# Kernel tuning notes

Hardware: AMD Instinct MI355X
Metric: run time of the kernel (lower is better)

The kernel has to match this reference:

```python
import jax, jax.numpy as jnp
import numpy as np

B, S, D, H = 8, 1024, 768, 12
DH = D // H
EPS = 1e-5
NEG = -1e9


def _layernorm(x, g, b):
    mu = jnp.mean(x, axis=-1, keepdims=True)
    var = jnp.mean((x - mu) ** 2, axis=-1, keepdims=True)
    return (x - mu) * jax.lax.rsqrt(var + EPS) * g + b


def setup_inputs() -> dict:
    key = jax.random.key(0)
    ks = jax.random.split(key, 20)
    sc = 0.02
    x = jax.random.normal(ks[0], (B, S, D), dtype=jnp.float32)
    src_mask = jax.random.randint(ks[1], (B, S), 0, 2) > 0
    # weights stored as (in, out): y = x @ W + b (same math as torch x @ W.T + b)
    Wq = jax.random.normal(ks[2], (D, D), jnp.float32) * sc
    bq = jnp.zeros((D,), jnp.float32)
    Wk = jax.random.normal(ks[3], (D, D), jnp.float32) * sc
    bk = jnp.zeros((D,), jnp.float32)
    Wv = jax.random.normal(ks[4], (D, D), jnp.float32) * sc
    bv = jnp.zeros((D,), jnp.float32)
    Wo = jax.random.normal(ks[5], (D, D), jnp.float32) * sc
    bo = jnp.zeros((D,), jnp.float32)
    g1 = jnp.ones((D,), jnp.float32)
    be1 = jnp.zeros((D,), jnp.float32)
    W1 = jax.random.normal(ks[6], (D, 2 * D), jnp.float32) * sc
    b1 = jnp.zeros((2 * D,), jnp.float32)
    W2 = jax.random.normal(ks[7], (2 * D, D), jnp.float32) * sc
    b2 = jnp.zeros((D,), jnp.float32)
    g2 = jnp.ones((D,), jnp.float32)
    be2 = jnp.zeros((D,), jnp.float32)
    return dict(x=x, src_mask=src_mask, Wq=Wq, bq=bq, Wk=Wk, bk=bk, Wv=Wv, bv=bv,
                Wo=Wo, bo=bo, g1=g1, be1=be1, W1=W1, b1=b1, W2=W2, b2=b2,
                g2=g2, be2=be2)


def reference(x, src_mask, Wq, bq, Wk, bk, Wv, bv, Wo, bo, g1, be1, W1, b1, W2, b2, g2, be2):
    # QKV projections, split into heads: [B, S, H, DH]
    q = (x @ Wq + bq).reshape(B, S, H, DH)
    k = (x @ Wk + bk).reshape(B, S, H, DH)
    v = (x @ Wv + bv).reshape(B, S, H, DH)
    # scores [B, H, S, S]; scale by sqrt(head_dim) as in original
    scores = jnp.einsum('bqhd,bkhd->bhqk', q, k) / np.sqrt(DH).astype(np.float32)
    # additive key mask broadcast over heads and queries
    mask = jnp.where(src_mask[:, None, None, :], 0.0, NEG).astype(scores.dtype)
    A = jax.nn.softmax(scores + mask, axis=-1)
    ctx = jnp.einsum('bhqk,bkhd->bqhd', A, v).reshape(B, S, D)
    attn_out = ctx @ Wo + bo + x
    h = _layernorm(attn_out, g1, be1)
    ff = jax.nn.relu(h @ W1 + b1) @ W2 + b2
    out = _layernorm(ff + h, g2, be2)
    return out
```

## Files before the change

kernel.cpp:

```cpp
#include <hip/hip_runtime.h>
#include <cstdint>
#include <cstddef>

typedef unsigned short u16;
typedef __attribute__((ext_vector_type(8))) __bf16 bf16x8;
typedef __attribute__((ext_vector_type(4))) float floatx4;

#define Bz 8
#define Sz 1024
#define Dz 768
#define Hz 12
#define DHz 64

__device__ __forceinline__ u16 f2b(float f) {
  unsigned u = __float_as_uint(f);
  return (u16)((u + 0x7fffu + ((u >> 16) & 1u)) >> 16);
}

__device__ __forceinline__ bf16x8 ld8(const u16* p) {
  union { uint4 u; bf16x8 b; } t;
  t.u = *reinterpret_cast<const uint4*>(p);
  return t.b;
}

__device__ __forceinline__ void load_lds16(const u16* g, u16* l) {
  __builtin_amdgcn_global_load_lds(
      (const __attribute__((address_space(1))) unsigned int*)g,
      (__attribute__((address_space(3))) unsigned int*)l, 16, 0, 0);
}

__global__ __launch_bounds__(256) void cvt4(const float* __restrict__ src,
                                            u16* __restrict__ dst, int n4) {
  int i = blockIdx.x * 256 + threadIdx.x;
  if (i >= n4) return;
  float4 v = reinterpret_cast<const float4*>(src)[i];
  union { u16 s[4]; uint2 u; } t;
  t.s[0] = f2b(v.x); t.s[1] = f2b(v.y); t.s[2] = f2b(v.z); t.s[3] = f2b(v.w);
  reinterpret_cast<uint2*>(dst)[i] = t.u;
}

__global__ __launch_bounds__(256)
void wtrans(const float* __restrict__ s0, const float* __restrict__ s1,
            const float* __restrict__ s2, u16* __restrict__ dst,
            int K, int N, int srcN) {
  __shared__ float T[32][33];
  const int tx = threadIdx.x & 31, ty = threadIdx.x >> 5;
  const int n0 = blockIdx.x * 32, k0 = blockIdx.y * 32;
  const int n = n0 + tx;
  const float* src = s0;
  int nn = n;
  if (s1 && n >= 1536) { src = s2; nn = n - 1536; }
  else if (s1 && n >= 768) { src = s1; nn = n - 768; }
#pragma unroll
  for (int i = 0; i < 4; ++i)
    T[ty + i * 8][tx] = src[(size_t)(k0 + ty + i * 8) * srcN + nn];
  __syncthreads();
#pragma unroll
  for (int i = 0; i < 4; ++i)
    dst[(size_t)(n0 + ty + i * 8) * K + k0 + tx] = f2b(T[tx][ty + i * 8]);
}

template <int EPI>
__global__ __launch_bounds__(256, 4)
void gemm_k(const u16* __restrict__ A, const u16* __restrict__ Bt,
            int M, int N, int K,
            const float* __restrict__ bias0, const float* __restrict__ bias1,
            const float* __restrict__ bias2, const float* __restrict__ resid,
            float* __restrict__ outF, u16* __restrict__ outB,
            u16* __restrict__ qO, u16* __restrict__ kO, u16* __restrict__ vtO) {
  __shared__ __align__(16) u16 As[2][128 * 32];
  __shared__ __align__(16) u16 Bs[2][128 * 32];
  const int tid = threadIdx.x;
  const int lane = tid & 63, wave = tid >> 6;
  const int l15 = lane & 15, quad = lane >> 4;
  const int m0 = blockIdx.y * 128, n0 = blockIdx.x * 128;
  const int wm = (wave >> 1) * 64, wn = (wave & 1) * 64;

  floatx4 acc[4][4];
#pragma unroll
  for (int i = 0; i < 4; ++i)
#pragma unroll
    for (int j = 0; j < 4; ++j) acc[i][j] = {0.f, 0.f, 0.f, 0.f};

  const int srow = lane >> 2;
  const int scol = (lane & 3) * 8;
  const u16* pA = A + (size_t)(m0 + wave * 32 + srow) * K + scol;
  const u16* pB = Bt + (size_t)(n0 + wave * 32 + srow) * K + scol;

#pragma unroll
  for (int j = 0; j < 2; ++j) {
    load_lds16(pA + (size_t)(j * 16) * K, &As[0][(wave * 2 + j) * 512]);
    load_lds16(pB + (size_t)(j * 16) * K, &Bs[0][(wave * 2 + j) * 512]);
  }

  const int NIT = K >> 5;
  for (int i = 0; i < NIT; ++i) {
    const int cur = i & 1;
    asm volatile("s_waitcnt vmcnt(0)" ::: "memory");
    __builtin_amdgcn_s_barrier();
    bf16x8 af[4], bf[4];
#pragma unroll
    for (int ii = 0; ii < 4; ++ii)
      af[ii] = ld8(&As[cur][(wm + ii * 16 + l15) * 32 + quad * 8]);
#pragma unroll
    for (int j = 0; j < 4; ++j)
      bf[j] = ld8(&Bs[cur][(wn + j * 16 + l15) * 32 + quad * 8]);
    __builtin_amdgcn_sched_barrier(0);
    if (i + 1 < NIT) {
      const int k1 = (i + 1) << 5;
#pragma unroll
      for (int j = 0; j < 2; ++j) {
        load_lds16(pA + (size_t)(j * 16) * K + k1, &As[cur ^ 1][(wave * 2 + j) * 512]);
        load_lds16(pB + (size_t)(j * 16) * K + k1, &Bs[cur ^ 1][(wave * 2 + j) * 512]);
      }
    }
#pragma unroll
    for (int ii = 0; ii < 4; ++ii)
#pragma unroll
      for (int j = 0; j < 4; ++j)
        acc[ii][j] = __builtin_amdgcn_mfma_f32_16x16x32_bf16(af[ii], bf[j],
                                                             acc[ii][j], 0, 0, 0);
  }

#pragma unroll
  for (int i = 0; i < 4; ++i) {
    int mbase = m0 + wm + i * 16 + quad * 4;
#pragma unroll
    for (int j = 0; j < 4; ++j) {
      int n = n0 + wn + j * 16 + l15;
#pragma unroll
      for (int r = 0; r < 4; ++r) {
        int mm = mbase + r;
        float v = acc[i][j][r];
        if (EPI == 0) {
          if (n < 768) {
            v += bias0[n];
            qO[(size_t)mm * 768 + n] = f2b(v);
          } else if (n < 1536) {
            v += bias1[n - 768];
            kO[(size_t)mm * 768 + (n - 768)] = f2b(v);
          } else {
            int d = n - 1536;
            v += bias2[d];
            int hh = d >> 6, dh = d & 63;
            int bb = mm >> 10, ss = mm & 1023;
            vtO[((size_t)(bb * Hz + hh) * DHz + dh) * Sz + ss] = f2b(v);
          }
        } else if (EPI == 1) {
          v += bias0[n] + resid[(size_t)mm * N + n];
          outF[(size_t)mm * N + n] = v;
        } else {
          v += bias0[n];
          v = fmaxf(v, 0.f);
          outB[(size_t)mm * N + n] = f2b(v);
        }
      }
    }
  }
}

__global__ __launch_bounds__(256, 3)
void attn_k(const u16* __restrict__ q, const u16* __restrict__ kbuf,
            const u16* __restrict__ vt, const int* __restrict__ mask,
            u16* __restrict__ ctx) {
  __shared__ float addend[Sz];
  __shared__ __align__(16) u16 Ks[128 * 64];
  __shared__ __align__(16) u16 Vs[64 * 128];
  __shared__ __align__(16) u16 P[4][16][132];
  const int tid = threadIdx.x;
  const int wave = tid >> 6, lane = tid & 63;
  const int l15 = lane & 15, quad = lane >> 4;
  const int bq = blockIdx.x;
  const int b = blockIdx.y / Hz, h = blockIdx.y % Hz;

  for (int s = tid; s < Sz; s += 256)
    addend[s] = mask[b * Sz + s] ? 0.f : -1e9f;

  const int qrow = bq * 64 + wave * 16 + l15;
  const u16* qp = q + (size_t)(b * Sz + qrow) * Dz + h * DHz;
  const bf16x8 fq0 = ld8(qp + quad * 8);
  const bf16x8 fq1 = ld8(qp + 32 + quad * 8);

  const int kchunk = (lane & 7) ^ (lane >> 3);
  const int l7 = l15 & 7;
  const int s0q = quad ^ l7;

  float m_l = -1e30f, l_l = 0.f;
  floatx4 o[4];
#pragma unroll
  for (int nt = 0; nt < 4; ++nt) o[nt] = {0.f, 0.f, 0.f, 0.f};

  const size_t vbase = (size_t)(b * Hz + h) * DHz * Sz;

  for (int kt = 0; kt < Sz / 128; ++kt) {
    __syncthreads();
#pragma unroll
    for (int j = 0; j < 4; ++j) {
      const int key = wave * 32 + j * 8 + (lane >> 3);
      load_lds16(kbuf + (size_t)(b * Sz + kt * 128 + key) * Dz + h * DHz +
                     kchunk * 8,
                 Ks + wave * 2048 + j * 512);
      const int dh = wave * 16 + j * 4 + (lane >> 4);
      const int vchunk = (lane & 15) ^ (dh & 7);
      load_lds16(vt + vbase + (size_t)dh * Sz + kt * 128 + vchunk * 8,
                 Vs + wave * 2048 + j * 512);
    }
    __syncthreads();

    floatx4 z[8];
#pragma unroll
    for (int t = 0; t < 8; ++t) {
      const int krow = t * 16 + l15;
      bf16x8 fk0 = ld8(&Ks[krow * 64 + s0q * 8]);
      bf16x8 fk1 = ld8(&Ks[krow * 64 + (s0q ^ 4) * 8]);
      floatx4 zz = {0.f, 0.f, 0.f, 0.f};
      zz = __builtin_amdgcn_mfma_f32_16x16x32_bf16(fk0, fq0, zz, 0, 0, 0);
      zz = __builtin_amdgcn_mfma_f32_16x16x32_bf16(fk1, fq1, zz, 0, 0, 0);
      const float4 ad =
          *reinterpret_cast<const float4*>(&addend[kt * 128 + t * 16 + quad * 4]);
      z[t][0] = zz[0] * 0.125f + ad.x;
      z[t][1] = zz[1] * 0.125f + ad.y;
      z[t][2] = zz[2] * 0.125f + ad.z;
      z[t][3] = zz[3] * 0.125f + ad.w;
    }
    float mx = z[0][0];
#pragma unroll
    for (int t = 0; t < 8; ++t)
#pragma unroll
      for (int r = 0; r < 4; ++r) mx = fmaxf(mx, z[t][r]);
    mx = fmaxf(mx, __shfl_xor(mx, 16, 64));
    mx = fmaxf(mx, __shfl_xor(mx, 32, 64));
    const float nm = fmaxf(m_l, mx);
    const float alpha = __expf(m_l - nm);
    m_l = nm;
    float su = 0.f;
#pragma unroll
    for (int t = 0; t < 8; ++t) {
      union { u16 s[4]; uint2 u; } pk;
#pragma unroll
      for (int r = 0; r < 4; ++r) {
        float p = __expf(z[t][r] - nm);
        su += p;
        pk.s[r] = f2b(p);
      }
      *reinterpret_cast<uint2*>(&P[wave][l15][t * 16 + quad * 4]) = pk.u;
    }
    su += __shfl_xor(su, 16, 64);
    su += __shfl_xor(su, 32, 64);
    l_l = l_l * alpha + su;
    float av[4];
#pragma unroll
    for (int r = 0; r < 4; ++r) av[r] = __shfl(alpha, quad * 4 + r, 64);
#pragma unroll
    for (int nt = 0; nt < 4; ++nt)
#pragma unroll
      for (int r = 0; r < 4; ++r) o[nt][r] *= av[r];
    bf16x8 ap[4];
#pragma unroll
    for (int c = 0; c < 4; ++c)
      ap[c] = ld8(&P[wave][l15][c * 32 + quad * 8]);
#pragma unroll
    for (int nt = 0; nt < 4; ++nt) {
#pragma unroll
      for (int c = 0; c < 4; ++c) {
        bf16x8 bv =
            ld8(&Vs[(nt * 16 + l15) * 128 + (((c * 4 + quad) ^ l7) * 8)]);
        o[nt] = __builtin_amdgcn_mfma_f32_16x16x32_bf16(ap[c], bv, o[nt], 0, 0, 0);
      }
    }
  }

  const float linv = 1.f / l_l;
  float lv[4];
#pragma unroll
  for (int r = 0; r < 4; ++r) lv[r] = __shfl(linv, quad * 4 + r, 64);
  const int qr = bq * 64 + wave * 16 + quad * 4;
#pragma unroll
  for (int nt = 0; nt < 4; ++nt)
#pragma unroll
    for (int r = 0; r < 4; ++r) {
      float v = o[nt][r] * lv[r];
      ctx[(size_t)(b * Sz + qr + r) * Dz + h * DHz + nt * 16 + l15] = f2b(v);
    }
}

__global__ __launch_bounds__(256)
void ln_k(const float* __restrict__ in, const float* __restrict__ g,
          const float* __restrict__ be, float* __restrict__ outF,
          u16* __restrict__ outB) {
  const int row = blockIdx.x;
  const float* x = in + (size_t)row * Dz;
  const int tid = threadIdx.x;
  float v0 = x[tid], v1 = x[tid + 256], v2 = x[tid + 512];
  float s = v0 + v1 + v2;
  float s2 = v0 * v0 + v1 * v1 + v2 * v2;
#pragma unroll
  for (int off = 1; off < 64; off <<= 1) {
    s += __shfl_xor(s, off, 64);
    s2 += __shfl_xor(s2, off, 64);
  }
  __shared__ float red[8];
  int wave = tid >> 6, lane = tid & 63;
  if (lane == 0) { red[wave] = s; red[4 + wave] = s2; }
  __syncthreads();
  s = red[0] + red[1] + red[2] + red[3];
  s2 = red[4] + red[5] + red[6] + red[7];
  const float mu = s * (1.f / 768.f);
  const float rstd = rsqrtf(s2 * (1.f / 768.f) - mu * mu + 1e-5f);
  float vv[3] = {v0, v1, v2};
#pragma unroll
  for (int e = 0; e < 3; ++e) {
    int col = tid + e * 256;
    float y = (vv[e] - mu) * rstd * g[col] + be[col];
    outF[(size_t)row * Dz + col] = y;
    if (outB) outB[(size_t)row * Dz + col] = f2b(y);
  }
}

extern "C" void kernel_launch(void* const* d_in, const int* in_sizes, int n_in,
                              void* d_out, int out_size, void* d_ws,
                              size_t ws_size, hipStream_t stream) {
  const float* x   = (const float*)d_in[0];
  const int*   msk = (const int*)d_in[1];
  const float* Wq  = (const float*)d_in[2];
  const float* bq  = (const float*)d_in[3];
  const float* Wk  = (const float*)d_in[4];
  const float* bk  = (const float*)d_in[5];
  const float* Wv  = (const float*)d_in[6];
  const float* bv  = (const float*)d_in[7];
  const float* Wo  = (const float*)d_in[8];
  const float* bo  = (const float*)d_in[9];
  const float* g1  = (const float*)d_in[10];
  const float* be1 = (const float*)d_in[11];
  const float* W1  = (const float*)d_in[12];
  const float* b1  = (const float*)d_in[13];
  const float* W2  = (const float*)d_in[14];
  const float* b2  = (const float*)d_in[15];
  const float* g2  = (const float*)d_in[16];
  const float* be2 = (const float*)d_in[17];
  float* out = (float*)d_out;

  char* ws = (char*)d_ws;
  u16*   xb    = (u16*)(ws + 0);
  u16*   wqkvb = (u16*)(ws + 12582912);
  u16*   wob   = (u16*)(ws + 16121856);
  u16*   w1b   = (u16*)(ws + 17301504);
  u16*   w2b   = (u16*)(ws + 19660800);
  u16*   qb    = (u16*)(ws + 22020096);
  u16*   kb    = (u16*)(ws + 34603008);
  u16*   vtb   = (u16*)(ws + 47185920);
  u16*   ctx   = (u16*)(ws + 59768832);
  float* att   = (float*)(ws + 72351744);
  float* hf    = (float*)(ws + 97517568);
  u16*   hb    = (u16*)(ws + 122683392);
  u16*   f1    = (u16*)(ws + 47185920);
  float* yy    = (float*)(ws + 22020096);

  cvt4<<<6291456 / 4 / 256, 256, 0, stream>>>(x, xb, 6291456 / 4);
  wtrans<<<dim3(2304 / 32, 768 / 32), 256, 0, stream>>>(Wq, Wk, Wv, wqkvb, 768,
                                                        2304, 768);
  wtrans<<<dim3(24, 24), 256, 0, stream>>>(Wo, nullptr, nullptr, wob, 768, 768,
                                           768);
  wtrans<<<dim3(48, 24), 256, 0, stream>>>(W1, nullptr, nullptr, w1b, 768, 1536,
                                           1536);
  wtrans<<<dim3(24, 48), 256, 0, stream>>>(W2, nullptr, nullptr, w2b, 1536, 768,
                                           768);

  gemm_k<0><<<dim3(2304 / 128, 8192 / 128), 256, 0, stream>>>(
      xb, wqkvb, 8192, 2304, 768, bq, bk, bv, nullptr, nullptr, nullptr, qb, kb,
      vtb);
  attn_k<<<dim3(Sz / 64, Bz * Hz), 256, 0, stream>>>(qb, kb, vtb, msk, ctx);
  gemm_k<1><<<dim3(768 / 128, 8192 / 128), 256, 0, stream>>>(
      ctx, wob, 8192, 768, 768, bo, nullptr, nullptr, x, att, nullptr, nullptr,
      nullptr, nullptr);
  ln_k<<<8192, 256, 0, stream>>>(att, g1, be1, hf, hb);
  gemm_k<2><<<dim3(1536 / 128, 8192 / 128), 256, 0, stream>>>(
      hb, w1b, 8192, 1536, 768, b1, nullptr, nullptr, nullptr, nullptr, f1,
      nullptr, nullptr, nullptr);
  gemm_k<1><<<dim3(768 / 128, 8192 / 128), 256, 0, stream>>>(
      f1, w2b, 8192, 768, 1536, b2, nullptr, nullptr, hf, yy, nullptr, nullptr,
      nullptr, nullptr);
  ln_k<<<8192, 256, 0, stream>>>(yy, g2, be2, out, nullptr);
}
```

Baseline: 387.9 us.

## Triple-buffer GEMM LDS tiles, swizzle LDS columns, and remap workgroups for XCD locality

The GEMM kernel moves from double to triple buffering. It prefetches two K-steps ahead and waits on a partial vmcnt, so global-to-LDS loads can overlap more MFMA work. LDS column chunks are XOR-swizzled on both the write and read side to cut bank conflicts. Both the GEMM and attention kernels remap the linear block id with a stride-8 swizzle so neighbouring tiles land on the same XCD and share L2. In exchange, LDS use per block rises and launch bounds drop to 3 blocks per CU, which may lower occupancy. The vmcnt(4) wait count must exactly match the number of outstanding loads issued per step.

```diff
diff --git a/kernel.cpp b/kernel.cpp
--- a/kernel.cpp
+++ b/kernel.cpp
@@ -61,19 +61,26 @@
 }
 
 template <int EPI>
-__global__ __launch_bounds__(256, 4)
+__global__ __launch_bounds__(256, 3)
 void gemm_k(const u16* __restrict__ A, const u16* __restrict__ Bt,
             int M, int N, int K,
             const float* __restrict__ bias0, const float* __restrict__ bias1,
             const float* __restrict__ bias2, const float* __restrict__ resid,
             float* __restrict__ outF, u16* __restrict__ outB,
             u16* __restrict__ qO, u16* __restrict__ kO, u16* __restrict__ vtO) {
-  __shared__ __align__(16) u16 As[2][128 * 32];
-  __shared__ __align__(16) u16 Bs[2][128 * 32];
+  __shared__ __align__(16) u16 As[3][128 * 32];
+  __shared__ __align__(16) u16 Bs[3][128 * 32];
   const int tid = threadIdx.x;
   const int lane = tid & 63, wave = tid >> 6;
   const int l15 = lane & 15, quad = lane >> 4;
-  const int m0 = blockIdx.y * 128, n0 = blockIdx.x * 128;
+
+  const int nx = gridDim.x;
+  const int nwg = nx * gridDim.y;
+  const int lin = blockIdx.y * nx + blockIdx.x;
+  const int swz = (lin & 7) * (nwg >> 3) + (lin >> 3);
+  const int bx = swz % nx, by = swz / nx;
+
+  const int m0 = by * 128, n0 = bx * 128;
   const int wm = (wave >> 1) * 64, wn = (wave & 1) * 64;
 
   floatx4 acc[4][4];
@@ -83,43 +90,50 @@
     for (int j = 0; j < 4; ++j) acc[i][j] = {0.f, 0.f, 0.f, 0.f};
 
   const int srow = lane >> 2;
-  const int scol = (lane & 3) * 8;
+  const int scol = (((lane & 3) ^ ((lane >> 3) & 3))) * 8;
   const u16* pA = A + (size_t)(m0 + wave * 32 + srow) * K + scol;
   const u16* pB = Bt + (size_t)(n0 + wave * 32 + srow) * K + scol;
 
 #pragma unroll
-  for (int j = 0; j < 2; ++j) {
-    load_lds16(pA + (size_t)(j * 16) * K, &As[0][(wave * 2 + j) * 512]);
-    load_lds16(pB + (size_t)(j * 16) * K, &Bs[0][(wave * 2 + j) * 512]);
-  }
+  for (int t = 0; t < 2; ++t)
+#pragma unroll
+    for (int j = 0; j < 2; ++j) {
+      load_lds16(pA + (size_t)(j * 16) * K + t * 32, &As[t][(wave * 2 + j) * 512]);
+      load_lds16(pB + (size_t)(j * 16) * K + t * 32, &Bs[t][(wave * 2 + j) * 512]);
+    }
 
   const int NIT = K >> 5;
+  const int rsw = (l15 >> 1) & 3;
+  int cur = 0;
   for (int i = 0; i < NIT; ++i) {
-    const int cur = i & 1;
-    asm volatile("s_waitcnt vmcnt(0)" ::: "memory");
+    if (i == NIT - 1) asm volatile("s_waitcnt vmcnt(0)" ::: "memory");
+    else              asm volatile("s_waitcnt vmcnt(4)" ::: "memory");
     __builtin_amdgcn_s_barrier();
     bf16x8 af[4], bf[4];
 #pragma unroll
     for (int ii = 0; ii < 4; ++ii)
-      af[ii] = ld8(&As[cur][(wm + ii * 16 + l15) * 32 + quad * 8]);
+      af[ii] = ld8(&As[cur][(wm + ii * 16 + l15) * 32 + (quad ^ rsw) * 8]);
 #pragma unroll
     for (int j = 0; j < 4; ++j)
-      bf[j] = ld8(&Bs[cur][(wn + j * 16 + l15) * 32 + quad * 8]);
+      bf[j] = ld8(&Bs[cur][(wn + j * 16 + l15) * 32 + (quad ^ rsw) * 8]);
     __builtin_amdgcn_sched_barrier(0);
-    if (i + 1 < NIT) {
-      const int k1 = (i + 1) << 5;
+    if (i + 2 < NIT) {
+      const int k2 = (i + 2) << 5;
+      int pf = cur + 2; if (pf >= 3) pf -= 3;
 #pragma unroll
       for (int j = 0; j < 2; ++j) {
-        load_lds16(pA + (size_t)(j * 16) * K + k1, &As[cur ^ 1][(wave * 2 + j) * 512]);
-        load_lds16(pB + (size_t)(j * 16) * K + k1, &Bs[cur ^ 1][(wave * 2 + j) * 512]);
+        load_lds16(pA + (size_t)(j * 16) * K + k2, &As[pf][(wave * 2 + j) * 512]);
+        load_lds16(pB + (size_t)(j * 16) * K + k2, &Bs[pf][(wave * 2 + j) * 512]);
       }
     }
+    __builtin_amdgcn_sched_barrier(0);
 #pragma unroll
     for (int ii = 0; ii < 4; ++ii)
 #pragma unroll
       for (int j = 0; j < 4; ++j)
         acc[ii][j] = __builtin_amdgcn_mfma_f32_16x16x32_bf16(af[ii], bf[j],
                                                              acc[ii][j], 0, 0, 0);
+    cur += 1; if (cur == 3) cur = 0;
   }
 
 #pragma unroll
@@ -170,8 +184,11 @@
   const int tid = threadIdx.x;
   const int wave = tid >> 6, lane = tid & 63;
   const int l15 = lane & 15, quad = lane >> 4;
-  const int bq = blockIdx.x;
-  const int b = blockIdx.y / Hz, h = blockIdx.y % Hz;
+  const int lin = blockIdx.y * 16 + blockIdx.x;
+  const int swzid = (lin & 7) * 192 + (lin >> 3);
+  const int bq = swzid & 15;
+  const int bh = swzid >> 4;
+  const int b = bh / Hz, h = bh - b * Hz;
 
   for (int s = tid; s < Sz; s += 256)
     addend[s] = mask[b * Sz + s] ? 0.f : -1e9f;
```

After: 368.8 us. 4.9% less time.
